# Kernel optimization log

Measured on AMD Instinct MI355X. Metric: run time of the kernel, lower is better.

The kernel has to match this reference:

```python
import jax, jax.numpy as jnp
import numpy as np

K = 96  # num_scales (conv kernel width)
PAD = K // 2


def setup_inputs() -> dict:
    key = jax.random.key(0)
    kx, kh, kl = jax.random.split(key, 3)
    x = jax.random.normal(kx, (64, 128, 4096), dtype=jnp.float32)
    h_w = jax.random.normal(kh, (1, 1, K), dtype=jnp.float32) * 0.1
    l_w = jax.random.normal(kl, (1, 1, K), dtype=jnp.float32) * 0.1
    return {"x": x, "h_w": h_w, "l_w": l_w}


def reference(x, h_w, l_w):
    # Original loops over channels applying the SAME Conv1d(1,1,K) to each
    # channel slice; this is exactly a depthwise conv with a shared filter.
    # Fold channels into the batch dim and run one conv per filter.
    B, C, T = x.shape
    xr = x.reshape(B * C, 1, T)  # [B*C, 1, T]

    def conv(w):
        # torch Conv1d is cross-correlation; lax conv matches (no kernel flip)
        y = jax.lax.conv_general_dilated(
            xr, w, window_strides=(1,), padding=[(PAD, PAD)],
            dimension_numbers=("NCH", "OIH", "NCH"))
        return y.reshape(B, C, -1)  # [B, C, T+1] for even K

    l_outs = conv(l_w)
    h_outs = conv(h_w)
    return (l_outs, h_outs)
```

## Files before the change

kernel.cpp:

```cpp
#include <hip/hip_runtime.h>


#define KW    96
#define PADW  48
#define T_IN  4096
#define T_OUT 4097
#define ROWS  8192
#define TT    2048
#define NTILE 16
#define BLOCK 256
#define NF4   544
#define XSH   (NF4 * 4)
#define BREG  2320

typedef __attribute__((ext_vector_type(8))) short short8;
typedef __attribute__((ext_vector_type(4))) float f32x4;

__device__ __forceinline__ unsigned short f2bf(float v) {
    unsigned u = __builtin_bit_cast(unsigned, v);
    u += 0x7FFFu + ((u >> 16) & 1u);
    return (unsigned short)(u >> 16);
}

__global__ __launch_bounds__(BLOCK) void lwt_init(
    const float* __restrict__ hw, const float* __restrict__ lw,
    unsigned short* __restrict__ ws)
{
    const int t = threadIdx.x;
    const int L = t >> 2, c = t & 3;
    const int n = L & 15, q = L >> 4;
    const int s = n & 7, f = n >> 3;
    const float* w = f ? hw : lw;
    unsigned short b[8];
    #pragma unroll
    for (int j = 0; j < 8; ++j) {
        const int k = 32 * c + 8 * q + j;
        const int kk = k - s;
        b[j] = (kk >= 0 && kk < KW) ? f2bf(w[kk]) : (unsigned short)0;
    }
    uint4 pk;
    pk.x = (unsigned)b[0] | ((unsigned)b[1] << 16);
    pk.y = (unsigned)b[2] | ((unsigned)b[3] << 16);
    pk.z = (unsigned)b[4] | ((unsigned)b[5] << 16);
    pk.w = (unsigned)b[6] | ((unsigned)b[7] << 16);
    ((uint4*)ws)[t] = pk;
}

__global__ __launch_bounds__(BLOCK) void lwt_main(
    const float* __restrict__ x,
    const float* __restrict__ hw,
    const float* __restrict__ lw,
    const unsigned short* __restrict__ ws,
    float* __restrict__ out_l,
    float* __restrict__ out_h)
{
    __shared__ alignas(16) unsigned short xs[XSH];
    __shared__ float bounce[2 * BREG];
    const int bid = blockIdx.x;
    const int tid = threadIdx.x;

    if (bid < ROWS * 2) {
        const int row = bid >> 1;
        const int T0  = (bid & 1) * TT;
        const float* xrow = x + (size_t)row * T_IN;

        for (int i = tid; i < NF4; i += BLOCK) {
            const int g = T0 - PADW + 4 * i;
            float4 v = make_float4(0.f, 0.f, 0.f, 0.f);
            if (g >= 0 && g < T_IN) v = *(const float4*)(xrow + g);
            ushort4 u;
            u.x = f2bf(v.x); u.y = f2bf(v.y); u.z = f2bf(v.z); u.w = f2bf(v.w);
            *(ushort4*)(xs + 4 * i) = u;
        }

        const int lane = tid & 63;
        const short8* wsB = (const short8*)ws;
        short8 bf0 = wsB[lane * 4 + 0];
        short8 bf1 = wsB[lane * 4 + 1];
        short8 bf2 = wsB[lane * 4 + 2];
        short8 bf3 = wsB[lane * 4 + 3];
        __syncthreads();

        const int wv = tid >> 6;
        const int m  = lane & 15;
        const int q  = lane >> 4;
        const int nD = lane & 15;
        const int sD = nD & 7;
        const int fD = nD >> 3;
        const short8* ap = (const short8*)xs;

        #pragma unroll
        for (int it = 0; it < 4; ++it) {
            const int tile = wv * 4 + it;
            const int ga0 = tile * 16 + m + q;
            f32x4 acc = {0.f, 0.f, 0.f, 0.f};
            acc = __builtin_amdgcn_mfma_f32_16x16x32_bf16(ap[ga0     ], bf0, acc, 0, 0, 0);
            acc = __builtin_amdgcn_mfma_f32_16x16x32_bf16(ap[ga0 +  4], bf1, acc, 0, 0, 0);
            acc = __builtin_amdgcn_mfma_f32_16x16x32_bf16(ap[ga0 +  8], bf2, acc, 0, 0, 0);
            acc = __builtin_amdgcn_mfma_f32_16x16x32_bf16(ap[ga0 + 12], bf3, acc, 0, 0, 0);
            #pragma unroll
            for (int r = 0; r < 4; ++r) {
                const int i0 = tile * 128 + 32 * q + 8 * r + sD;
                bounce[fD * BREG + i0 + (i0 >> 3)] = acc[r];
            }
        }
        __syncthreads();

        const size_t ob = (size_t)row * T_OUT + T0;
        #pragma unroll
        for (int rep = 0; rep < TT / BLOCK; ++rep) {
            const int i = tid + rep * BLOCK;
            out_l[ob + i] = bounce[i + (i >> 3)];
        }
        #pragma unroll
        for (int rep = 0; rep < TT / BLOCK; ++rep) {
            const int i = tid + rep * BLOCK;
            out_h[ob + i] = bounce[BREG + i + (i >> 3)];
        }
    } else {
        const int r = (bid - ROWS * 2) * BLOCK + tid;
        if (r < ROWS) {
            const float* xp = x + (size_t)r * T_IN + (T_OUT - 1 - PADW);
            float al = 0.f, ah = 0.f;
            #pragma unroll
            for (int k = 0; k < PADW; ++k) {
                const float xv = xp[k];
                al = fmaf(xv, lw[k], al);
                ah = fmaf(xv, hw[k], ah);
            }
            const size_t o = (size_t)r * T_OUT + (T_OUT - 1);
            out_l[o] = al;
            out_h[o] = ah;
        }
    }
}

extern "C" void kernel_launch(void* const* d_in, const int* in_sizes, int n_in,
                              void* d_out, int out_size, void* d_ws, size_t ws_size,
                              hipStream_t stream) {
    const float* x  = (const float*)d_in[0];
    const float* hw = (const float*)d_in[1];
    const float* lw = (const float*)d_in[2];
    float* out_l = (float*)d_out;
    float* out_h = out_l + (size_t)ROWS * T_OUT;
    unsigned short* wsB = (unsigned short*)d_ws;

    lwt_init<<<1, BLOCK, 0, stream>>>(hw, lw, wsB);
    const int grid = ROWS * 2 + ROWS / BLOCK;
    lwt_main<<<grid, BLOCK, 0, stream>>>(x, hw, lw, wsB, out_l, out_h);
}
```

Before: 367.2 us.

## Process whole row per block with per-wave phased bounce and interleaved stores

Each block now handles a full 4096-sample row instead of half, so there are half as many blocks and less redundant halo loading. The shared-memory bounce buffer becomes a small per-wave region reused across four phases. Each wave writes its outputs right after computing them, with no block-wide barrier. Launch bounds request 4 blocks per CU, and the smaller LDS footprint should help occupancy. In exchange, each block does more serial work and the grid has fewer blocks.

After: 367.4 us. No clear change (+0.1%).

```diff
diff --git a/kernel.cpp b/kernel.cpp
--- a/kernel.cpp
+++ b/kernel.cpp
@@ -6,12 +6,10 @@
 #define T_IN  4096
 #define T_OUT 4097
 #define ROWS  8192
-#define TT    2048
-#define NTILE 16
 #define BLOCK 256
-#define NF4   544
+#define NF4   1056
 #define XSH   (NF4 * 4)
-#define BREG  2320
+#define BNC   320
 
 typedef __attribute__((ext_vector_type(8))) short short8;
 typedef __attribute__((ext_vector_type(4))) float f32x4;
@@ -46,7 +44,7 @@
     ((uint4*)ws)[t] = pk;
 }
 
-__global__ __launch_bounds__(BLOCK) void lwt_main(
+__global__ __launch_bounds__(BLOCK, 4) void lwt_main(
     const float* __restrict__ x,
     const float* __restrict__ hw,
     const float* __restrict__ lw,
@@ -55,70 +53,70 @@
     float* __restrict__ out_h)
 {
     __shared__ alignas(16) unsigned short xs[XSH];
-    __shared__ float bounce[2 * BREG];
+    __shared__ float bounce[4][2][BNC];
     const int bid = blockIdx.x;
     const int tid = threadIdx.x;
 
-    if (bid < ROWS * 2) {
-        const int row = bid >> 1;
-        const int T0  = (bid & 1) * TT;
-        const float* xrow = x + (size_t)row * T_IN;
+    if (bid < ROWS) {
+        const int lane = tid & 63;
 
+        const short8* wsB = (const short8*)ws;
+        short8 bf0 = wsB[lane * 4 + 0];
+        short8 bf1 = wsB[lane * 4 + 1];
+        short8 bf2 = wsB[lane * 4 + 2];
+        short8 bf3 = wsB[lane * 4 + 3];
+
+        const float* xrow = x + (size_t)bid * T_IN;
         for (int i = tid; i < NF4; i += BLOCK) {
-            const int g = T0 - PADW + 4 * i;
+            const int g = 4 * i - PADW;
             float4 v = make_float4(0.f, 0.f, 0.f, 0.f);
             if (g >= 0 && g < T_IN) v = *(const float4*)(xrow + g);
             ushort4 u;
             u.x = f2bf(v.x); u.y = f2bf(v.y); u.z = f2bf(v.z); u.w = f2bf(v.w);
             *(ushort4*)(xs + 4 * i) = u;
         }
-
-        const int lane = tid & 63;
-        const short8* wsB = (const short8*)ws;
-        short8 bf0 = wsB[lane * 4 + 0];
-        short8 bf1 = wsB[lane * 4 + 1];
-        short8 bf2 = wsB[lane * 4 + 2];
-        short8 bf3 = wsB[lane * 4 + 3];
         __syncthreads();
 
         const int wv = tid >> 6;
         const int m  = lane & 15;
         const int q  = lane >> 4;
-        const int nD = lane & 15;
-        const int sD = nD & 7;
-        const int fD = nD >> 3;
+        const int sD = m & 7;
+        const int fD = m >> 3;
         const short8* ap = (const short8*)xs;
+        float* bw = &bounce[wv][fD][0];
+        const size_t ob = (size_t)bid * T_OUT + (size_t)wv * 1024;
 
-        #pragma unroll
-        for (int it = 0; it < 4; ++it) {
-            const int tile = wv * 4 + it;
-            const int ga0 = tile * 16 + m + q;
-            f32x4 acc = {0.f, 0.f, 0.f, 0.f};
-            acc = __builtin_amdgcn_mfma_f32_16x16x32_bf16(ap[ga0     ], bf0, acc, 0, 0, 0);
-            acc = __builtin_amdgcn_mfma_f32_16x16x32_bf16(ap[ga0 +  4], bf1, acc, 0, 0, 0);
-            acc = __builtin_amdgcn_mfma_f32_16x16x32_bf16(ap[ga0 +  8], bf2, acc, 0, 0, 0);
-            acc = __builtin_amdgcn_mfma_f32_16x16x32_bf16(ap[ga0 + 12], bf3, acc, 0, 0, 0);
+        #pragma unroll 1
+        for (int ph = 0; ph < 4; ++ph) {
             #pragma unroll
-            for (int r = 0; r < 4; ++r) {
-                const int i0 = tile * 128 + 32 * q + 8 * r + sD;
-                bounce[fD * BREG + i0 + (i0 >> 3)] = acc[r];
+            for (int it = 0; it < 2; ++it) {
+                const int tile = wv * 8 + ph * 2 + it;
+                const int ga0 = tile * 16 + m + q;
+                f32x4 acc = {0.f, 0.f, 0.f, 0.f};
+                acc = __builtin_amdgcn_mfma_f32_16x16x32_bf16(ap[ga0     ], bf0, acc, 0, 0, 0);
+                acc = __builtin_amdgcn_mfma_f32_16x16x32_bf16(ap[ga0 +  4], bf1, acc, 0, 0, 0);
+                acc = __builtin_amdgcn_mfma_f32_16x16x32_bf16(ap[ga0 +  8], bf2, acc, 0, 0, 0);
+                acc = __builtin_amdgcn_mfma_f32_16x16x32_bf16(ap[ga0 + 12], bf3, acc, 0, 0, 0);
+                #pragma unroll
+                for (int r = 0; r < 4; ++r) {
+                    const int i0 = it * 128 + 32 * q + 8 * r + sD;
+                    bw[i0 + 8 * (i0 >> 5)] = acc[r];
+                }
+            }
+            const int tb = ph * 256;
+            #pragma unroll
+            for (int p = 0; p < 4; ++p) {
+                const int i = lane + 64 * p;
+                out_l[ob + tb + i] = bounce[wv][0][i + 8 * (i >> 5)];
+            }
+            #pragma unroll
+            for (int p = 0; p < 4; ++p) {
+                const int i = lane + 64 * p;
+                out_h[ob + tb + i] = bounce[wv][1][i + 8 * (i >> 5)];
             }
         }
-        __syncthreads();
-
-        const size_t ob = (size_t)row * T_OUT + T0;
-        #pragma unroll
-        for (int rep = 0; rep < TT / BLOCK; ++rep) {
-            const int i = tid + rep * BLOCK;
-            out_l[ob + i] = bounce[i + (i >> 3)];
-        }
-        #pragma unroll
-        for (int rep = 0; rep < TT / BLOCK; ++rep) {
-            const int i = tid + rep * BLOCK;
-            out_h[ob + i] = bounce[BREG + i + (i >> 3)];
-        }
     } else {
-        const int r = (bid - ROWS * 2) * BLOCK + tid;
+        const int r = (bid - ROWS) * BLOCK + tid;
         if (r < ROWS) {
             const float* xp = x + (size_t)r * T_IN + (T_OUT - 1 - PADW);
             float al = 0.f, ah = 0.f;
@@ -146,6 +144,6 @@
     unsigned short* wsB = (unsigned short*)d_ws;
 
     lwt_init<<<1, BLOCK, 0, stream>>>(hw, lw, wsB);
-    const int grid = ROWS * 2 + ROWS / BLOCK;
+    const int grid = ROWS + ROWS / BLOCK;
     lwt_main<<<grid, BLOCK, 0, stream>>>(x, hw, lw, wsB, out_l, out_h);
 }
```
